# Kernel optimization log

Hardware: AMD Instinct MI355X
Metric: run time of the kernel (lower is better)

## Reference

```python
import jax, jax.numpy as jnp
import numpy as np

K = 7           # kernel_size
GROUPS = 16     # channels // group_channels = 256 // 16
GC = 16         # group_channels
BN_EPS = 1e-5


def setup_inputs() -> dict:
    key = jax.random.key(0)
    ks = jax.random.split(key, 6)
    B, C, H, W = 4, 256, 64, 64
    cr = C // 4                      # reduction_ratio = 4
    k2g = K * K * GROUPS             # conv2 out channels = 784
    return {
        "feature_map": jax.random.normal(ks[0], (B, C, H, W), jnp.float32),
        "guide_map":   jax.random.normal(ks[1], (B, C, H, W), jnp.float32),
        "w1": jax.random.normal(ks[2], (cr, C), jnp.float32) * 0.05,
        "bn_gamma": jnp.ones((cr,), jnp.float32),
        "bn_beta":  jnp.zeros((cr,), jnp.float32),
        "bn_mean":  jax.random.normal(ks[3], (cr,), jnp.float32) * 0.1,
        "bn_var":   jax.random.uniform(ks[4], (cr,), jnp.float32, 0.5, 1.5),
        "w2": jax.random.normal(ks[5], (k2g, cr), jnp.float32) * 0.05,
        "b2": jnp.zeros((k2g,), jnp.float32),
    }


def reference(feature_map, guide_map, w1, bn_gamma, bn_beta, bn_mean, bn_var, w2, b2):
    b, c, h, w = feature_map.shape
    # conv1 (1x1) + BN (inference stats) + ReLU
    x = jnp.einsum("oc,bchw->bohw", w1, guide_map)
    inv = bn_gamma / jnp.sqrt(bn_var + BN_EPS)
    x = x * inv[None, :, None, None] + (bn_beta - bn_mean * inv)[None, :, None, None]
    x = jax.nn.relu(x)
    # conv2 (1x1): dynamic per-pixel kernel weights -> [b, groups, k^2, h, w]
    weight = jnp.einsum("oc,bchw->bohw", w2, x) + b2[None, :, None, None]
    weight = weight.reshape(b, GROUPS, K * K, h, w)
    # unfold feature_map (same padding, stride 1) -> [b, c, k^2, h, w]
    pad = (K - 1) // 2
    fp = jnp.pad(feature_map, ((0, 0), (0, 0), (pad, pad), (pad, pad)))
    patches = jnp.stack(
        [fp[:, :, i:i + h, j:j + w] for i in range(K) for j in range(K)], axis=2
    )
    patches = patches.reshape(b, GROUPS, GC, K * K, h, w)
    # dynamic weighted aggregation over kernel positions, then residual
    out = jnp.einsum("bgkhw,bgckhw->bgchw", weight, patches)
    return out.reshape(b, c, h, w) + feature_map
```

## Files before the change

kernel.cpp:

```cpp
#include <hip/hip_runtime.h>

#define BN_EPS 1e-5f

typedef __bf16 bf16_t;
typedef __bf16 bf16x8 __attribute__((ext_vector_type(8)));
typedef __bf16 bf16x4 __attribute__((ext_vector_type(4)));
typedef __bf16 bf16x2 __attribute__((ext_vector_type(2)));
typedef float  floatx4 __attribute__((ext_vector_type(4)));

#define MFMA16(a, b, c) __builtin_amdgcn_mfma_f32_16x16x32_bf16((a), (b), (c), 0, 0, 0)

#define XT_OFF 0

#define GTP 264
#define W1P 264

__global__ __launch_bounds__(256) void conv1_k(
    const float* __restrict__ guide, const float* __restrict__ w1,
    const float* __restrict__ gamma, const float* __restrict__ beta,
    const float* __restrict__ mean,  const float* __restrict__ var,
    bf16_t* __restrict__ xT)
{
    __shared__ __attribute__((aligned(16))) bf16_t gTs[64 * GTP];
    __shared__ __attribute__((aligned(16))) bf16_t w1s[64 * W1P];
    const int b = blockIdx.x >> 6, h = blockIdx.x & 63;
    const int t = threadIdx.x;

#pragma unroll
    for (int i = 0; i < 16; ++i) {
        const int idx = i * 256 + t;
        const int o = idx >> 6, cq = idx & 63;
        const float inv = gamma[o] * rsqrtf(var[o] + BN_EPS);
        const float4 v = *(const float4*)(w1 + o * 256 + cq * 4);
        bf16_t* d = &w1s[o * W1P + cq * 4];
        d[0] = (bf16_t)(v.x * inv); d[1] = (bf16_t)(v.y * inv);
        d[2] = (bf16_t)(v.z * inv); d[3] = (bf16_t)(v.w * inv);
    }
    const float* gsrc = guide + (size_t)b * 256 * 4096 + h * 64;
#pragma unroll
    for (int i = 0; i < 32; ++i) {
        const int idx = i * 256 + t;
        const int c2 = idx >> 6, p = idx & 63;
        const float g0 = gsrc[(size_t)(2 * c2) * 4096 + p];
        const float g1 = gsrc[(size_t)(2 * c2 + 1) * 4096 + p];
        bf16x2 pk; pk[0] = (bf16_t)g0; pk[1] = (bf16_t)g1;
        *(bf16x2*)&gTs[p * GTP + 2 * c2] = pk;
    }
    __syncthreads();

    const int wv = t >> 6, ln = t & 63, l15 = ln & 15, q = ln >> 4;
    floatx4 acc[4] = {};
    const bf16_t* ap = &w1s[(wv * 16 + l15) * W1P];
#pragma unroll
    for (int ks = 0; ks < 8; ++ks) {
        const bf16x8 a = *(const bf16x8*)(ap + ks * 32 + q * 8);
#pragma unroll
        for (int nt = 0; nt < 4; ++nt) {
            const bf16x8 bb = *(const bf16x8*)&gTs[(nt * 16 + l15) * GTP + ks * 32 + q * 8];
            acc[nt] = MFMA16(a, bb, acc[nt]);
        }
    }
    float bi[4];
#pragma unroll
    for (int j = 0; j < 4; ++j) {
        const int o = wv * 16 + q * 4 + j;
        const float iv = gamma[o] * rsqrtf(var[o] + BN_EPS);
        bi[j] = beta[o] - mean[o] * iv;
    }
#pragma unroll
    for (int nt = 0; nt < 4; ++nt) {
        const int p = nt * 16 + l15;
        bf16x4 v;
#pragma unroll
        for (int j = 0; j < 4; ++j) v[j] = (bf16_t)fmaxf(acc[nt][j] + bi[j], 0.f);
        *(bf16x4*)(xT + ((size_t)(b * 64 + h) * 64 + p) * 64 + wv * 16 + q * 4) = v;
    }
}

#define FSR 72
#define FSC 576
#define WGP 136

__global__ __launch_bounds__(256) void fused_k(
    const bf16_t* __restrict__ xT, const float* __restrict__ w2,
    const float* __restrict__ b2,  const float* __restrict__ feat,
    float* __restrict__ out)
{
    __shared__ __attribute__((aligned(16))) float  fs[16 * FSC];
    __shared__ __attribute__((aligned(16))) bf16_t wgs[49 * WGP];

    const int g = blockIdx.x & 15;
    const int rest = blockIdx.x >> 4;
    const int b = rest >> 5, hp = rest & 31;
    const int h0 = hp * 2;
    const int t = threadIdx.x;
    const int wv = t >> 6, ln = t & 63, l15 = ln & 15, q = ln >> 4;

#pragma unroll
    for (int i = 0; i < 9; ++i) {
        const int u = i * 256 + t;
        const int c = u / 144, rem = u - c * 144;
        const int rr = rem / 18, qq = rem - rr * 18;
        const int hh = h0 - 3 + rr;
        float4 v = {0.f, 0.f, 0.f, 0.f};
        if (qq >= 1 && qq <= 16 && hh >= 0 && hh < 64)
            v = *(const float4*)(feat + ((size_t)(b * 256 + g * 16 + c) * 64 + hh) * 64 + (qq - 1) * 4);
        *(float4*)&fs[c * FSC + rr * FSR + qq * 4] = v;
    }

    {
        floatx4 acc[4][2] = {};
        const bf16_t* brow = xT + ((size_t)(b * 64 + h0) * 64 + wv * 32) * 64;
#pragma unroll
        for (int ks = 0; ks < 2; ++ks) {
            bf16x8 bfr[2];
            bfr[0] = *(const bf16x8*)(brow + l15 * 64 + ks * 32 + q * 8);
            bfr[1] = *(const bf16x8*)(brow + (16 + l15) * 64 + ks * 32 + q * 8);
#pragma unroll
            for (int mt = 0; mt < 4; ++mt) {
                int row = mt * 16 + l15; if (row > 48) row = 48;
                const float* wp = w2 + (size_t)(g * 49 + row) * 64 + ks * 32 + q * 8;
                const float4 a0 = *(const float4*)(wp);
                const float4 a1 = *(const float4*)(wp + 4);
                bf16x8 a;
                a[0] = (bf16_t)a0.x; a[1] = (bf16_t)a0.y; a[2] = (bf16_t)a0.z; a[3] = (bf16_t)a0.w;
                a[4] = (bf16_t)a1.x; a[5] = (bf16_t)a1.y; a[6] = (bf16_t)a1.z; a[7] = (bf16_t)a1.w;
                acc[mt][0] = MFMA16(a, bfr[0], acc[mt][0]);
                acc[mt][1] = MFMA16(a, bfr[1], acc[mt][1]);
            }
        }
#pragma unroll
        for (int mt = 0; mt < 4; ++mt) {
#pragma unroll
            for (int j = 0; j < 4; ++j) {
                const int k = mt * 16 + q * 4 + j;
                if (k < 49) {
                    const float bias = b2[g * 49 + k];
                    wgs[k * WGP + wv * 32 + l15]      = (bf16_t)(acc[mt][0][j] + bias);
                    wgs[k * WGP + wv * 32 + 16 + l15] = (bf16_t)(acc[mt][1][j] + bias);
                }
            }
        }
    }
    __syncthreads();

    const int wq = t & 15, r = (t >> 4) & 1, cp = t >> 5;
    const int w0 = wq * 4;
    const int ch0 = cp * 2;

    float acc[2][4] = {};
#pragma unroll
    for (int di = 0; di < 7; ++di) {
        const int ri = r + di;
        float f0[12], f1[12];
        {
            const float* p0 = &fs[ch0 * FSC + ri * FSR + w0];
            const float* p1 = p0 + FSC;
#pragma unroll
            for (int qj = 0; qj < 3; ++qj) {
                const floatx4 a = *(const floatx4*)(p0 + qj * 4);
                const floatx4 bq = *(const floatx4*)(p1 + qj * 4);
#pragma unroll
                for (int j = 0; j < 4; ++j) { f0[qj * 4 + j] = a[j]; f1[qj * 4 + j] = bq[j]; }
            }
        }
        const bf16_t* wrow = &wgs[(di * 7) * WGP + r * 64 + w0];
#pragma unroll
        for (int dj = 0; dj < 7; ++dj) {
            const bf16x4 wb = *(const bf16x4*)(wrow + dj * WGP);
#pragma unroll
            for (int x = 0; x < 4; ++x) {
                const float wf = (float)wb[x];
                acc[0][x] = fmaf(wf, f0[x + dj + 1], acc[0][x]);
                acc[1][x] = fmaf(wf, f1[x + dj + 1], acc[1][x]);
            }
        }
    }

#pragma unroll
    for (int c = 0; c < 2; ++c) {
        const floatx4 res = *(const floatx4*)&fs[(ch0 + c) * FSC + (r + 3) * FSR + 4 + w0];
        const size_t ob = ((size_t)(b * 256 + g * 16 + ch0 + c) * 64 + h0 + r) * 64 + w0;
        float4 o;
        o.x = acc[c][0] + res[0]; o.y = acc[c][1] + res[1];
        o.z = acc[c][2] + res[2]; o.w = acc[c][3] + res[3];
        *(float4*)(out + ob) = o;
    }
}

extern "C" void kernel_launch(void* const* d_in, const int* in_sizes, int n_in,
                              void* d_out, int out_size, void* d_ws, size_t ws_size,
                              hipStream_t stream) {
    const float* feature = (const float*)d_in[0];
    const float* guide   = (const float*)d_in[1];
    const float* w1      = (const float*)d_in[2];
    const float* gamma   = (const float*)d_in[3];
    const float* beta    = (const float*)d_in[4];
    const float* mean    = (const float*)d_in[5];
    const float* var     = (const float*)d_in[6];
    const float* w2      = (const float*)d_in[7];
    const float* b2      = (const float*)d_in[8];
    float* out = (float*)d_out;

    bf16_t* xT = (bf16_t*)((char*)d_ws + XT_OFF);

    conv1_k<<<256, 256, 0, stream>>>(guide, w1, gamma, beta, mean, var, xT);
    fused_k<<<2048, 256, 0, stream>>>(xT, w2, b2, feature, out);
}
```

Baseline: 122.6 us.

## Store feature tile in LDS as bf16 and load residual from global

```diff
diff --git a/kernel.cpp b/kernel.cpp
--- a/kernel.cpp
+++ b/kernel.cpp
@@ -77,16 +77,16 @@
     }
 }
 
-#define FSR 72
-#define FSC 576
+#define FSR2 72
+#define FSC2 576
 #define WGP 136
 
-__global__ __launch_bounds__(256) void fused_k(
+__global__ __launch_bounds__(256, 5) void fused_k(
     const bf16_t* __restrict__ xT, const float* __restrict__ w2,
     const float* __restrict__ b2,  const float* __restrict__ feat,
     float* __restrict__ out)
 {
-    __shared__ __attribute__((aligned(16))) float  fs[16 * FSC];
+    __shared__ __attribute__((aligned(16))) bf16_t fs2[16 * FSC2];
     __shared__ __attribute__((aligned(16))) bf16_t wgs[49 * WGP];
 
     const int g = blockIdx.x & 15;
@@ -96,16 +96,32 @@
     const int t = threadIdx.x;
     const int wv = t >> 6, ln = t & 63, l15 = ln & 15, q = ln >> 4;
 
-#pragma unroll
-    for (int i = 0; i < 9; ++i) {
+    const int wq = t & 15, r = (t >> 4) & 1, cp = t >> 5;
+    const int w0 = wq * 4;
+    const int ch0 = cp * 2;
+
+    float4 res[2];
+#pragma unroll
+    for (int c = 0; c < 2; ++c)
+        res[c] = *(const float4*)(feat + ((size_t)(b * 256 + g * 16 + ch0 + c) * 64 + h0 + r) * 64 + w0);
+
+#pragma unroll
+    for (int i = 0; i < 5; ++i) {
         const int u = i * 256 + t;
-        const int c = u / 144, rem = u - c * 144;
-        const int rr = rem / 18, qq = rem - rr * 18;
-        const int hh = h0 - 3 + rr;
-        float4 v = {0.f, 0.f, 0.f, 0.f};
-        if (qq >= 1 && qq <= 16 && hh >= 0 && hh < 64)
-            v = *(const float4*)(feat + ((size_t)(b * 256 + g * 16 + c) * 64 + hh) * 64 + (qq - 1) * 4);
-        *(float4*)&fs[c * FSC + rr * FSR + qq * 4] = v;
+        if (u < 1152) {
+            const int c = u / 72, rem = u - c * 72;
+            const int rr = rem / 9, j = rem - rr * 9;
+            const int hh = h0 - 3 + rr;
+            const float* rp = feat + ((size_t)(b * 256 + g * 16 + c) * 64 + hh) * 64;
+            float4 lo = {0.f, 0.f, 0.f, 0.f}, hi = {0.f, 0.f, 0.f, 0.f};
+            const bool hok = (hh >= 0) && (hh < 64);
+            if (hok && j >= 1) lo = *(const float4*)(rp + 8 * j - 4);
+            if (hok && j <= 7) hi = *(const float4*)(rp + 8 * j);
+            bf16x8 v;
+            v[0] = (bf16_t)lo.x; v[1] = (bf16_t)lo.y; v[2] = (bf16_t)lo.z; v[3] = (bf16_t)lo.w;
+            v[4] = (bf16_t)hi.x; v[5] = (bf16_t)hi.y; v[6] = (bf16_t)hi.z; v[7] = (bf16_t)hi.w;
+            *(bf16x8*)&fs2[c * FSC2 + rr * FSR2 + j * 8] = v;
+        }
     }
 
     {
@@ -144,24 +160,23 @@
     }
     __syncthreads();
 
-    const int wq = t & 15, r = (t >> 4) & 1, cp = t >> 5;
-    const int w0 = wq * 4;
-    const int ch0 = cp * 2;
-
     float acc[2][4] = {};
 #pragma unroll
     for (int di = 0; di < 7; ++di) {
         const int ri = r + di;
         float f0[12], f1[12];
         {
-            const float* p0 = &fs[ch0 * FSC + ri * FSR + w0];
-            const float* p1 = p0 + FSC;
+            const bf16_t* p0 = &fs2[ch0 * FSC2 + ri * FSR2 + w0];
+            const bf16_t* p1 = p0 + FSC2;
 #pragma unroll
             for (int qj = 0; qj < 3; ++qj) {
-                const floatx4 a = *(const floatx4*)(p0 + qj * 4);
-                const floatx4 bq = *(const floatx4*)(p1 + qj * 4);
-#pragma unroll
-                for (int j = 0; j < 4; ++j) { f0[qj * 4 + j] = a[j]; f1[qj * 4 + j] = bq[j]; }
+                const bf16x4 a = *(const bf16x4*)(p0 + qj * 4);
+                const bf16x4 bq = *(const bf16x4*)(p1 + qj * 4);
+#pragma unroll
+                for (int j = 0; j < 4; ++j) {
+                    f0[qj * 4 + j] = (float)a[j];
+                    f1[qj * 4 + j] = (float)bq[j];
+                }
             }
         }
         const bf16_t* wrow = &wgs[(di * 7) * WGP + r * 64 + w0];
@@ -179,11 +194,10 @@
 
 #pragma unroll
     for (int c = 0; c < 2; ++c) {
-        const floatx4 res = *(const floatx4*)&fs[(ch0 + c) * FSC + (r + 3) * FSR + 4 + w0];
         const size_t ob = ((size_t)(b * 256 + g * 16 + ch0 + c) * 64 + h0 + r) * 64 + w0;
         float4 o;
-        o.x = acc[c][0] + res[0]; o.y = acc[c][1] + res[1];
-        o.z = acc[c][2] + res[2]; o.w = acc[c][3] + res[3];
+        o.x = acc[c][0] + res[c].x; o.y = acc[c][1] + res[c].y;
+        o.z = acc[c][2] + res[c].z; o.w = acc[c][3] + res[c].w;
         *(float4*)(out + ob) = o;
     }
 }
```

Result: slower. 170.9 us (+39.4%).
